# Kernel optimization log

Hardware: AMD Instinct MI355X
Metric: run time of the kernel (lower is better)

## Reference

```python
import jax, jax.numpy as jnp
import numpy as np

N_NODES = 50000
N_EDGES = 1600000
IN_DIM = 128
OUT_DIM = 32
N_HEADS = 4


def setup_inputs() -> dict:
    key = jax.random.key(0)
    k_x, k_e, k_w, k_a = jax.random.split(key, 4)
    x = jax.random.normal(k_x, (N_NODES, IN_DIM), dtype=jnp.float32)
    edge_index = jax.random.randint(k_e, (N_EDGES, 2), 0, N_NODES, dtype=jnp.int64)
    # Xavier-uniform-like init scales
    w_bound = np.sqrt(6.0 / (IN_DIM + OUT_DIM)).astype(np.float32)
    a_bound = np.sqrt(6.0 / (N_HEADS + 2 * OUT_DIM)).astype(np.float32)
    weight = jax.random.uniform(k_w, (N_HEADS, IN_DIM, OUT_DIM), dtype=jnp.float32,
                                minval=-w_bound, maxval=w_bound)
    attn = jax.random.uniform(k_a, (N_HEADS, 2 * OUT_DIM), dtype=jnp.float32,
                              minval=-a_bound, maxval=a_bound)
    return {"x": x, "edge_index": edge_index, "weight": weight, "attn": attn}


def reference(x, edge_index, weight, attn):
    # x: [N, in_dim]; edge_index: [E, 2]; weight: [H, in, out]; attn: [H, 2*out]
    num_nodes = x.shape[0]
    out_dim = weight.shape[2]
    src = edge_index[:, 0]
    dst = edge_index[:, 1]

    # Per-head linear transform: [N, H, out]
    Wh = jnp.einsum('ni,hio->nho', x, weight)
    Wh_src = Wh[src]  # [E, H, out]
    Wh_dst = Wh[dst]  # [E, H, out]

    a_src = attn[:, :out_dim]   # [H, out]
    a_dst = attn[:, out_dim:]   # [H, out]
    # Edge scores: [E, H]
    e = jnp.einsum('eho,ho->eh', Wh_src, a_src) + jnp.einsum('eho,ho->eh', Wh_dst, a_dst)
    e = jax.nn.leaky_relu(e, negative_slope=0.2)

    # Segment softmax over incoming edges of each dst node
    max_per_dst = jax.ops.segment_max(e, dst, num_segments=num_nodes)  # [N, H]
    max_per_dst = jnp.where(jnp.isfinite(max_per_dst), max_per_dst, 0.0)
    exp_e = jnp.exp(e - max_per_dst[dst])                               # [E, H]
    sum_per_dst = jax.ops.segment_sum(exp_e, dst, num_segments=num_nodes)  # [N, H]
    alpha = exp_e / (sum_per_dst[dst] + 1e-9)                           # [E, H]
    # Dropout is identity in eval mode.

    # Weighted scatter-add aggregation: [N, H, out]
    out = jax.ops.segment_sum(alpha[:, :, None] * Wh_src, dst, num_segments=num_nodes)
    h = out.reshape(num_nodes, -1)  # concat heads -> [N, H*out]
    return h, alpha
```

## Files before the change

### kernel.cpp

```cpp
#include <hip/hip_runtime.h>
#include <hip/hip_bf16.h>
#include <math.h>

#define N_NODES 50000
#define N_EDGES 1600000
#define IN_DIM  128
#define OUT_DIM 32
#define N_HEADS 4
#define WH_DIM  (N_HEADS * OUT_DIM)
#define CAP     128
#define NB_SCAN 196
#define NPASS   4
#define WIN     (N_NODES / NPASS)
#define NCH2    32
#define SEGCAP  410000
#define UNROLL  16
#define EPB     (256 * UNROLL)
#define NB_CVT  391
#define NB_WH   782
#define SFLAG   (1 << 30)

typedef __attribute__((ext_vector_type(8))) short short8;
typedef __attribute__((ext_vector_type(4))) float floatx4;

__device__ __forceinline__ short f2bf(float v) {
    __hip_bfloat16 b = __float2bfloat16(v);
    return *reinterpret_cast<short*>(&b);
}
__device__ __forceinline__ float lrelu(float v) {
    return v > 0.0f ? v : 0.2f * v;
}

__device__ __forceinline__ void load_edge(const void* eidx, int is32, int e,
                                          int& s, int& d) {
    if (is32) {
        const int2 v = ((const int2*)eidx)[e];
        s = v.x; d = v.y;
    } else {
        const longlong2 v = ((const longlong2*)eidx)[e];
        s = (int)v.x; d = (int)v.y;
    }
}

__global__ __launch_bounds__(256) void k_prep0(
        const float* __restrict__ weight, const float* __restrict__ attn,
        short* __restrict__ bsw_pre, int* __restrict__ win_cnt,
        int* __restrict__ bsum) {
    __shared__ float ubuf[128 * 8];
    const int t = threadIdx.x;
    if (t < NPASS) win_cnt[t] = 0;
    if (t < NB_SCAN) bsum[t] = 0;
    {
        int c = t & 7, k0 = t >> 3;
        int h = c & 3;
        const float* ap = attn + h * 64 + (c >> 2) * 32;
        for (int k = k0; k < 128; k += 32) {
            const float* wp = weight + h * (IN_DIM * OUT_DIM) + k * OUT_DIM;
            float u = 0.f;
#pragma unroll
            for (int o = 0; o < 32; o += 4) {
                float4 wv = *(const float4*)(wp + o);
                float4 av = *(const float4*)(ap + o);
                u += wv.x * av.x + wv.y * av.y + wv.z * av.z + wv.w * av.w;
            }
            ubuf[k * 8 + c] = u;
        }
    }
    __syncthreads();
    for (int f = t; f < 128 * 128; f += 256) {
        int k = f >> 7, c = f & 127;
        float w = weight[(c >> 5) * (IN_DIM * OUT_DIM) + k * OUT_DIM + (c & 31)];
        int kc = k >> 5, quad = (k >> 3) & 3, j = k & 7;
        bsw_pre[((kc * 9 + (c >> 4)) * 64 + quad * 16 + (c & 15)) * 8 + j] =
            f2bf(w);
    }
    for (int f = t; f < 128 * 16; f += 256) {
        int k = f >> 4, c = f & 15;
        float w = (c < 8) ? ubuf[k * 8 + c] : 0.f;
        int kc = k >> 5, quad = (k >> 3) & 3, j = k & 7;
        bsw_pre[((kc * 9 + 8) * 64 + quad * 16 + c) * 8 + j] = f2bf(w);
    }
}

union CvtWhSmem {
    struct {
        int s_is32;
        int wcnt[NPASS][UNROLL][4];
        int pb[NPASS][UNROLL][4];
        int bw[NPASS];
    } c;
    struct {
        short xsw[4 * 4 * 64 * 8];
        short bsw[4 * 9 * 64 * 8];
    } w;
};

__global__ __launch_bounds__(256) void k_cvtwh(
        const void* __restrict__ eidx, const float* __restrict__ x,
        const short* __restrict__ bsw_pre,
        int* __restrict__ win_cnt, int* __restrict__ win_sd,
        __hip_bfloat16* __restrict__ Wh16, float* __restrict__ sb16) {
    __shared__ CvtWhSmem sm;
    const int t = threadIdx.x;

    if (blockIdx.x < NB_CVT) {
        const int wv = t >> 6, lane = t & 63;
        if (t < 64) {
            int hi = ((const int*)eidx)[2 * (t * 25000) + 1];
            unsigned long long b = __ballot(hi != 0);
            if (t == 0) sm.c.s_is32 = (b != 0ULL) ? 1 : 0;
        }
        __syncthreads();
        const int is32 = sm.c.s_is32;
        const int e0 = blockIdx.x * EPB;
        int sg[UNROLL], dg[UNROLL];
#pragma unroll
        for (int i = 0; i < UNROLL; ++i) {
            const int e = e0 + i * 256 + t;
            int s = 0, d = -1;
            if (e < N_EDGES) load_edge(eidx, is32, e, s, d);
            sg[i] = s; dg[i] = d;
            const int w = (d >= 0) ? (d / WIN) : -1;
            const unsigned long long m0 = __ballot(w == 0);
            const unsigned long long m1 = __ballot(w == 1);
            const unsigned long long m2 = __ballot(w == 2);
            const unsigned long long m3 = __ballot(w == 3);
            if (lane == 0) {
                sm.c.wcnt[0][i][wv] = __popcll(m0);
                sm.c.wcnt[1][i][wv] = __popcll(m1);
                sm.c.wcnt[2][i][wv] = __popcll(m2);
                sm.c.wcnt[3][i][wv] = __popcll(m3);
            }
        }
        __syncthreads();
        if (t < NPASS) {
            int run = 0;
            for (int i = 0; i < UNROLL; ++i)
                for (int v = 0; v < 4; ++v) {
                    sm.c.pb[t][i][v] = run;
                    run += sm.c.wcnt[t][i][v];
                }
            sm.c.bw[t] = atomicAdd(&win_cnt[t], run);
        }
        __syncthreads();
        const unsigned long long mlt = (1ULL << lane) - 1ULL;
#pragma unroll
        for (int i = 0; i < UNROLL; ++i) {
            const int d = dg[i];
            const int w = (d >= 0) ? (d / WIN) : -1;
            const unsigned long long m0 = __ballot(w == 0);
            const unsigned long long m1 = __ballot(w == 1);
            const unsigned long long m2 = __ballot(w == 2);
            const unsigned long long m3 = __ballot(w == 3);
            if (w >= 0) {
                const unsigned long long mw = (w == 0) ? m0 : (w == 1) ? m1
                                            : (w == 2) ? m2 : m3;
                const int rank = __popcll(mw & mlt);
                const int p = sm.c.bw[w] + sm.c.pb[w][i][wv] + rank;
                if (p < SEGCAP)
                    win_sd[w * SEGCAP + p] = sg[i] | ((d - w * WIN) << 17);
            }
        }
    } else {
        const int nb = (blockIdx.x - NB_CVT) * 64;
        for (int f = t; f < 4 * 9 * 64; f += 256)
            *(short8*)&sm.w.bsw[f * 8] = *(const short8*)&bsw_pre[f * 8];
        for (int f = t; f < 64 * 32; f += 256) {
            int n = f >> 5, k = (f & 31) * 4;
            int ng = nb + n; if (ng > N_NODES - 1) ng = N_NODES - 1;
            float4 v = *(const float4*)(x + (size_t)ng * IN_DIM + k);
            int wg = n >> 4, m = n & 15, kc = k >> 5, quad = (k >> 3) & 3,
                j = k & 7;
            short4 sv = make_short4(f2bf(v.x), f2bf(v.y), f2bf(v.z), f2bf(v.w));
            *(short4*)&sm.w.xsw[(((wg * 4 + kc) * 64) + quad * 16 + m) * 8 + j]
                = sv;
        }
        __syncthreads();
        const int wg = t >> 6, lane = t & 63;
        floatx4 acc[9];
#pragma unroll
        for (int i = 0; i < 9; ++i) acc[i] = (floatx4){0.f, 0.f, 0.f, 0.f};
#pragma unroll
        for (int kc = 0; kc < 4; ++kc) {
            short8 a = *(short8*)&sm.w.xsw[((wg * 4 + kc) * 64 + lane) * 8];
#pragma unroll
            for (int cg = 0; cg < 9; ++cg) {
                short8 b = *(short8*)&sm.w.bsw[((kc * 9 + cg) * 64 + lane) * 8];
                acc[cg] = __builtin_amdgcn_mfma_f32_16x16x32_bf16(a, b, acc[cg],
                                                                  0, 0, 0);
            }
        }
        const int col = lane & 15, quad = lane >> 4;
#pragma unroll
        for (int r = 0; r < 4; ++r) {
            int n = nb + wg * 16 + quad * 4 + r;
            if (n >= N_NODES) continue;
#pragma unroll
            for (int cg = 0; cg < 8; ++cg)
                Wh16[(size_t)n * WH_DIM + cg * 16 + col] =
                    __float2bfloat16(acc[cg][r]);
            if (col < 8) sb16[(size_t)n * 16 + col] = acc[8][r];
        }
    }
}

__global__ __launch_bounds__(1024) void k_hist(
        const int* __restrict__ win_cnt, const int* __restrict__ win_sd,
        int* __restrict__ hist) {
    __shared__ int hbin[WIN];
    const int c = blockIdx.x, w = blockIdx.y;
    for (int i = threadIdx.x; i < WIN; i += 1024) hbin[i] = 0;
    __syncthreads();
    const int cw = win_cnt[w];
    const int ce = (cw + NCH2 - 1) / NCH2;
    const int lo = c * ce;
    const int hi = min(lo + ce, cw);
    for (int i = lo + threadIdx.x; i < hi; i += 1024) {
        unsigned u = ((unsigned)win_sd[w * SEGCAP + i]) >> 17;
        if (u < WIN) atomicAdd(&hbin[u], 1);
    }
    __syncthreads();
    for (int i = threadIdx.x; i < WIN; i += 1024)
        hist[(w * NCH2 + c) * WIN + i] = hbin[i];
}

__global__ __launch_bounds__(256) void k_scanbase(
        int* __restrict__ bsum, int* __restrict__ hist,
        int* __restrict__ noff) {
    __shared__ int sh[256];
    const int t = threadIdx.x;
    const int b = blockIdx.x;
    const int i = b * 256 + t;
    int v = 0;
    if (i < N_NODES) {
        const int w = i / WIN, bin = i % WIN;
        for (int c = 0; c < NCH2; ++c) v += hist[(w * NCH2 + c) * WIN + bin];
    }
    sh[t] = v;
    __syncthreads();
    for (int d = 1; d < 256; d <<= 1) {
        int u = (t >= d) ? sh[t - d] : 0;
        __syncthreads();
        sh[t] += u;
        __syncthreads();
    }
    const int myex = sh[t] - v;
    if (t == 255) atomicExch(&bsum[b], sh[255] | SFLAG);
    __syncthreads();
    int bvv = 0;
    if (t < NB_SCAN) {
        int xx;
        do { xx = atomicAdd(&bsum[t], 0); } while (!(xx & SFLAG));
        bvv = xx & ~SFLAG;
    }
    sh[t] = bvv;
    __syncthreads();
    for (int d = 1; d < 256; d <<= 1) {
        int u = (t >= d) ? sh[t - d] : 0;
        __syncthreads();
        sh[t] += u;
        __syncthreads();
    }
    const int exb = (b == 0) ? 0 : sh[b - 1];
    if (b == 0 && t == 0) noff[N_NODES] = N_EDGES;
    if (i >= N_NODES) return;
    int run = myex + exb;
    noff[i] = run;
    const int w = i / WIN, bin = i % WIN;
    for (int c = 0; c < NCH2; ++c) {
        const int idx = (w * NCH2 + c) * WIN + bin;
        int t0 = hist[idx];
        hist[idx] = run;
        run += t0;
    }
}

__global__ __launch_bounds__(1024) void k_scatter(
        const int* __restrict__ win_cnt, const int* __restrict__ win_sd,
        const int* __restrict__ hist, int* __restrict__ csr) {
    __shared__ int pos[WIN];
    const int c = blockIdx.x, w = blockIdx.y;
    for (int i = threadIdx.x; i < WIN; i += 1024)
        pos[i] = hist[(w * NCH2 + c) * WIN + i];
    __syncthreads();
    const int cw = win_cnt[w];
    const int ce = (cw + NCH2 - 1) / NCH2;
    const int lo = c * ce;
    const int hi = min(lo + ce, cw);
    for (int i = lo + threadIdx.x; i < hi; i += 1024) {
        const int pk = win_sd[w * SEGCAP + i];
        const int s = pk & 0x1FFFF;
        const unsigned u = ((unsigned)pk) >> 17;
        if (u < WIN) {
            int p = atomicAdd(&pos[u], 1);
            csr[p] = s;
        }
    }
}

__global__ __launch_bounds__(256) void k_node(
        const int* __restrict__ noff,
        const int* __restrict__ csr, float* __restrict__ sb16,
        const __hip_bfloat16* __restrict__ Wh16,
        float* __restrict__ out_h) {
    __shared__ int    sbuf[4][CAP];
    __shared__ float4 e4b[4][CAP];
    const int wv = threadIdx.x >> 6;
    const int t  = threadIdx.x & 63;
    const int n  = blockIdx.x * 4 + wv;
    const int beg = noff[n];
    const int end = noff[n + 1];
    const int deg = end - beg;

    const float4 sd = *(const float4*)(sb16 + (size_t)n * 16 + 4);

    float4 sum = {0.f, 0.f, 0.f, 0.f};
    for (int l = t; l < deg; l += 64) {
        int s = csr[beg + l];
        float4 ss = *(const float4*)(sb16 + (size_t)s * 16);
        float4 ex;
        ex.x = __expf(lrelu(ss.x + sd.x));
        ex.y = __expf(lrelu(ss.y + sd.y));
        ex.z = __expf(lrelu(ss.z + sd.z));
        ex.w = __expf(lrelu(ss.w + sd.w));
        if (l < CAP) { sbuf[wv][l] = s; e4b[wv][l] = ex; }
        sum.x += ex.x; sum.y += ex.y; sum.z += ex.z; sum.w += ex.w;
    }
#pragma unroll
    for (int o = 32; o; o >>= 1) {
        sum.x += __shfl_xor(sum.x, o);
        sum.y += __shfl_xor(sum.y, o);
        sum.z += __shfl_xor(sum.z, o);
        sum.w += __shfl_xor(sum.w, o);
    }
    float4 inv;
    inv.x = 1.0f / (sum.x + 1e-9f); inv.y = 1.0f / (sum.y + 1e-9f);
    inv.z = 1.0f / (sum.z + 1e-9f); inv.w = 1.0f / (sum.w + 1e-9f);
    if (t == 0) *(float4*)(sb16 + (size_t)n * 16 + 8) = inv;

    const int esl = t >> 4;
    const int dsl = t & 15;
    const int h   = dsl >> 2;
    const float invh = (h == 0) ? inv.x : (h == 1) ? inv.y
                     : (h == 2) ? inv.z : inv.w;
    const float sdh  = (h == 0) ? sd.x : (h == 1) ? sd.y
                     : (h == 2) ? sd.z : sd.w;
    float acc0 = 0.f, acc1 = 0.f, acc2 = 0.f, acc3 = 0.f;
    float acc4 = 0.f, acc5 = 0.f, acc6 = 0.f, acc7 = 0.f;
    if (deg <= CAP) {
        const int sPad = sbuf[wv][0];
        for (int jb = 0; jb < deg; jb += 16) {
            int   sg[4];
            float ag[4];
#pragma unroll
            for (int g = 0; g < 4; ++g) {
                const int idx = jb + g * 4 + esl;
                sg[g] = sPad;
                ag[g] = 0.f;
                if (idx < deg) {
                    sg[g] = sbuf[wv][idx];
                    ag[g] = ((const float*)&e4b[wv][idx])[h];
                }
            }
            uint4 w0 = *(const uint4*)(Wh16 + (size_t)sg[0] * WH_DIM + dsl * 8);
            uint4 w1 = *(const uint4*)(Wh16 + (size_t)sg[1] * WH_DIM + dsl * 8);
            uint4 w2 = *(const uint4*)(Wh16 + (size_t)sg[2] * WH_DIM + dsl * 8);
            uint4 w3 = *(const uint4*)(Wh16 + (size_t)sg[3] * WH_DIM + dsl * 8);
#define ACC8(W, A)                                                            \
            acc0 += (A) * __uint_as_float((W).x << 16);                       \
            acc1 += (A) * __uint_as_float((W).x & 0xffff0000u);               \
            acc2 += (A) * __uint_as_float((W).y << 16);                       \
            acc3 += (A) * __uint_as_float((W).y & 0xffff0000u);               \
            acc4 += (A) * __uint_as_float((W).z << 16);                       \
            acc5 += (A) * __uint_as_float((W).z & 0xffff0000u);               \
            acc6 += (A) * __uint_as_float((W).w << 16);                       \
            acc7 += (A) * __uint_as_float((W).w & 0xffff0000u)
            ACC8(w0, ag[0]);
            ACC8(w1, ag[1]);
            ACC8(w2, ag[2]);
            ACC8(w3, ag[3]);
#undef ACC8
        }
    } else {
        for (int jb = 0; jb < deg; jb += 4) {
            const int idx = jb + esl;
            float a = 0.f;
            int s = sbuf[wv][0];
            if (idx < deg) {
                if (idx < CAP) {
                    s = sbuf[wv][idx];
                    a = ((const float*)&e4b[wv][idx])[h];
                } else {
                    s = csr[beg + idx];
                    a = __expf(lrelu(sb16[(size_t)s * 16 + h] + sdh));
                }
            }
            const uint4 w = *(const uint4*)(Wh16 + (size_t)s * WH_DIM + dsl * 8);
            acc0 += a * __uint_as_float(w.x << 16);
            acc1 += a * __uint_as_float(w.x & 0xffff0000u);
            acc2 += a * __uint_as_float(w.y << 16);
            acc3 += a * __uint_as_float(w.y & 0xffff0000u);
            acc4 += a * __uint_as_float(w.z << 16);
            acc5 += a * __uint_as_float(w.z & 0xffff0000u);
            acc6 += a * __uint_as_float(w.w << 16);
            acc7 += a * __uint_as_float(w.w & 0xffff0000u);
        }
    }
    acc0 += __shfl_xor(acc0, 16); acc0 += __shfl_xor(acc0, 32);
    acc1 += __shfl_xor(acc1, 16); acc1 += __shfl_xor(acc1, 32);
    acc2 += __shfl_xor(acc2, 16); acc2 += __shfl_xor(acc2, 32);
    acc3 += __shfl_xor(acc3, 16); acc3 += __shfl_xor(acc3, 32);
    acc4 += __shfl_xor(acc4, 16); acc4 += __shfl_xor(acc4, 32);
    acc5 += __shfl_xor(acc5, 16); acc5 += __shfl_xor(acc5, 32);
    acc6 += __shfl_xor(acc6, 16); acc6 += __shfl_xor(acc6, 32);
    acc7 += __shfl_xor(acc7, 16); acc7 += __shfl_xor(acc7, 32);
    if (t < 16) {
        float* op = out_h + (size_t)n * WH_DIM + dsl * 8;
        float4 o0 = {acc0 * invh, acc1 * invh, acc2 * invh, acc3 * invh};
        float4 o1 = {acc4 * invh, acc5 * invh, acc6 * invh, acc7 * invh};
        *(float4*)op = o0;
        *(float4*)(op + 4) = o1;
    }
}

__global__ __launch_bounds__(256) void k_alpha(
        const void* __restrict__ eidx,
        const float* __restrict__ sb16, float* __restrict__ ebuf) {
    __shared__ int s_is32;
    const int t = threadIdx.x;
    if (t < 64) {
        int hi = ((const int*)eidx)[2 * (t * 25000) + 1];
        unsigned long long b = __ballot(hi != 0);
        if (t == 0) s_is32 = (b != 0ULL) ? 1 : 0;
    }
    __syncthreads();
    const int e = blockIdx.x * 256 + t;
    int s, d;
    load_edge(eidx, s_is32, e, s, d);
    float4 ss = *(const float4*)(sb16 + (size_t)s * 16);
    float4 sd = *(const float4*)(sb16 + (size_t)d * 16 + 4);
    float4 iv = *(const float4*)(sb16 + (size_t)d * 16 + 8);
    float4 a;
    a.x = __expf(lrelu(ss.x + sd.x)) * iv.x;
    a.y = __expf(lrelu(ss.y + sd.y)) * iv.y;
    a.z = __expf(lrelu(ss.z + sd.z)) * iv.z;
    a.w = __expf(lrelu(ss.w + sd.w)) * iv.w;
    *(float4*)(ebuf + (size_t)e * 4) = a;
}

extern "C" void kernel_launch(void* const* d_in, const int* in_sizes, int n_in,
                              void* d_out, int out_size, void* d_ws, size_t ws_size,
                              hipStream_t stream) {
    const float* x      = (const float*)d_in[0];
    const void*  eidx   = d_in[1];
    const float* weight = (const float*)d_in[2];
    const float* attn   = (const float*)d_in[3];

    float* out   = (float*)d_out;
    float* out_h = out;
    float* ebuf  = out + (size_t)N_NODES * WH_DIM;

    char* ws = (char*)d_ws;
    int*   win_cnt = (int*)ws;
    int*   bsum    = (int*)(ws + 64);
    short* bsw_pre = (short*)(ws + 1024);
    int*   noff    = (int*)(ws + 37952);
    int*   win_sd  = (int*)(ws + 238016);
    int*   hist    = (int*)(ws + 6798080);
    int*   csr     = (int*)(ws + 13198144);
    __hip_bfloat16* Wh16 = (__hip_bfloat16*)(ws + 19598208);
    float* sb16    = (float*)(ws + 32398272);

    k_prep0<<<1, 256, 0, stream>>>(weight, attn, bsw_pre, win_cnt, bsum);
    k_cvtwh<<<NB_CVT + NB_WH, 256, 0, stream>>>(eidx, x, bsw_pre, win_cnt,
                                                win_sd, Wh16, sb16);
    dim3 hg(NCH2, NPASS);
    k_hist<<<hg, 1024, 0, stream>>>(win_cnt, win_sd, hist);
    k_scanbase<<<NB_SCAN, 256, 0, stream>>>(bsum, hist, noff);
    k_scatter<<<hg, 1024, 0, stream>>>(win_cnt, win_sd, hist, csr);
    k_node<<<N_NODES / 4, 256, 0, stream>>>(noff, csr, sb16, Wh16, out_h);
    k_alpha<<<N_EDGES / 256, 256, 0, stream>>>(eidx, sb16, ebuf);
}
```

Before: 253.5 us.

## Fuse histogram, scan and scatter into one persistent kernel with grid barriers

Merges the three counting-sort kernels (histogram, scan, scatter) into a single 128-block persistent kernel that uses atomic global barriers between phases, removing two kernel launches and their gaps. The scan now uses 1024-wide blocks and a simple serial prefix over 49 block sums. The weight-to-bf16 swizzle in the prep kernel is spread across 16 blocks instead of one. The grid barrier relies on all 128 blocks being co-resident, which holds on this GPU but is not guaranteed in general. It also adds spin-wait overhead.

```diff
diff --git a/kernel.cpp b/kernel.cpp
--- a/kernel.cpp
+++ b/kernel.cpp
@@ -9,7 +9,6 @@
 #define N_HEADS 4
 #define WH_DIM  (N_HEADS * OUT_DIM)
 #define CAP     128
-#define NB_SCAN 196
 #define NPASS   4
 #define WIN     (N_NODES / NPASS)
 #define NCH2    32
@@ -18,7 +17,9 @@
 #define EPB     (256 * UNROLL)
 #define NB_CVT  391
 #define NB_WH   782
-#define SFLAG   (1 << 30)
+#define NB_SORT (NCH2 * NPASS)
+#define NB_P2   49
+#define NB_PREP 16
 
 typedef __attribute__((ext_vector_type(8))) short short8;
 typedef __attribute__((ext_vector_type(4))) float floatx4;
@@ -42,14 +43,34 @@
     }
 }
 
+__device__ __forceinline__ void gbar(int* bar, int idx) {
+    __syncthreads();
+    if (threadIdx.x == 0) {
+        __threadfence();
+        atomicAdd(&bar[idx], 1);
+        while (atomicAdd(&bar[idx], 0) < NB_SORT) {}
+        __threadfence();
+    }
+    __syncthreads();
+}
+
 __global__ __launch_bounds__(256) void k_prep0(
         const float* __restrict__ weight, const float* __restrict__ attn,
         short* __restrict__ bsw_pre, int* __restrict__ win_cnt,
-        int* __restrict__ bsum) {
+        int* __restrict__ bar) {
     __shared__ float ubuf[128 * 8];
     const int t = threadIdx.x;
+    const int b = blockIdx.x;
+    for (int f = b * 1024 + t; f < (b + 1) * 1024; f += 256) {
+        int k = f >> 7, c = f & 127;
+        float w = weight[(c >> 5) * (IN_DIM * OUT_DIM) + k * OUT_DIM + (c & 31)];
+        int kc = k >> 5, quad = (k >> 3) & 3, j = k & 7;
+        bsw_pre[((kc * 9 + (c >> 4)) * 64 + quad * 16 + (c & 15)) * 8 + j] =
+            f2bf(w);
+    }
+    if (b != 0) return;
     if (t < NPASS) win_cnt[t] = 0;
-    if (t < NB_SCAN) bsum[t] = 0;
+    if (t < 8) bar[t] = 0;
     {
         int c = t & 7, k0 = t >> 3;
         int h = c & 3;
@@ -67,13 +88,6 @@
         }
     }
     __syncthreads();
-    for (int f = t; f < 128 * 128; f += 256) {
-        int k = f >> 7, c = f & 127;
-        float w = weight[(c >> 5) * (IN_DIM * OUT_DIM) + k * OUT_DIM + (c & 31)];
-        int kc = k >> 5, quad = (k >> 3) & 3, j = k & 7;
-        bsw_pre[((kc * 9 + (c >> 4)) * 64 + quad * 16 + (c & 15)) * 8 + j] =
-            f2bf(w);
-    }
     for (int f = t; f < 128 * 16; f += 256) {
         int k = f >> 4, c = f & 15;
         float w = (c < 8) ? ubuf[k * 8 + c] : 0.f;
@@ -204,96 +218,84 @@
     }
 }
 
-__global__ __launch_bounds__(1024) void k_hist(
+__global__ __launch_bounds__(1024) void k_sort(
         const int* __restrict__ win_cnt, const int* __restrict__ win_sd,
-        int* __restrict__ hist) {
-    __shared__ int hbin[WIN];
-    const int c = blockIdx.x, w = blockIdx.y;
-    for (int i = threadIdx.x; i < WIN; i += 1024) hbin[i] = 0;
+        int* __restrict__ hist, int* __restrict__ bsum2,
+        int* __restrict__ noff, int* __restrict__ csr, int* __restrict__ bar) {
+    __shared__ int lds[WIN];
+    __shared__ int xb;
+    const int bid = blockIdx.x;
+    const int t = threadIdx.x;
+    const int c = bid & (NCH2 - 1), w = bid >> 5;
+    for (int i = t; i < WIN; i += 1024) lds[i] = 0;
     __syncthreads();
     const int cw = win_cnt[w];
     const int ce = (cw + NCH2 - 1) / NCH2;
-    const int lo = c * ce;
-    const int hi = min(lo + ce, cw);
-    for (int i = lo + threadIdx.x; i < hi; i += 1024) {
+    const int lo = c * ce, hi = min(lo + ce, cw);
+    for (int i = lo + t; i < hi; i += 1024) {
         unsigned u = ((unsigned)win_sd[w * SEGCAP + i]) >> 17;
-        if (u < WIN) atomicAdd(&hbin[u], 1);
-    }
-    __syncthreads();
-    for (int i = threadIdx.x; i < WIN; i += 1024)
-        hist[(w * NCH2 + c) * WIN + i] = hbin[i];
-}
-
-__global__ __launch_bounds__(256) void k_scanbase(
-        int* __restrict__ bsum, int* __restrict__ hist,
-        int* __restrict__ noff) {
-    __shared__ int sh[256];
-    const int t = threadIdx.x;
-    const int b = blockIdx.x;
-    const int i = b * 256 + t;
-    int v = 0;
-    if (i < N_NODES) {
-        const int w = i / WIN, bin = i % WIN;
-        for (int c = 0; c < NCH2; ++c) v += hist[(w * NCH2 + c) * WIN + bin];
-    }
-    sh[t] = v;
-    __syncthreads();
-    for (int d = 1; d < 256; d <<= 1) {
-        int u = (t >= d) ? sh[t - d] : 0;
-        __syncthreads();
-        sh[t] += u;
-        __syncthreads();
-    }
-    const int myex = sh[t] - v;
-    if (t == 255) atomicExch(&bsum[b], sh[255] | SFLAG);
-    __syncthreads();
-    int bvv = 0;
-    if (t < NB_SCAN) {
-        int xx;
-        do { xx = atomicAdd(&bsum[t], 0); } while (!(xx & SFLAG));
-        bvv = xx & ~SFLAG;
-    }
-    sh[t] = bvv;
-    __syncthreads();
-    for (int d = 1; d < 256; d <<= 1) {
-        int u = (t >= d) ? sh[t - d] : 0;
-        __syncthreads();
-        sh[t] += u;
-        __syncthreads();
-    }
-    const int exb = (b == 0) ? 0 : sh[b - 1];
-    if (b == 0 && t == 0) noff[N_NODES] = N_EDGES;
-    if (i >= N_NODES) return;
-    int run = myex + exb;
-    noff[i] = run;
-    const int w = i / WIN, bin = i % WIN;
-    for (int c = 0; c < NCH2; ++c) {
-        const int idx = (w * NCH2 + c) * WIN + bin;
-        int t0 = hist[idx];
-        hist[idx] = run;
-        run += t0;
-    }
-}
-
-__global__ __launch_bounds__(1024) void k_scatter(
-        const int* __restrict__ win_cnt, const int* __restrict__ win_sd,
-        const int* __restrict__ hist, int* __restrict__ csr) {
-    __shared__ int pos[WIN];
-    const int c = blockIdx.x, w = blockIdx.y;
-    for (int i = threadIdx.x; i < WIN; i += 1024)
-        pos[i] = hist[(w * NCH2 + c) * WIN + i];
-    __syncthreads();
-    const int cw = win_cnt[w];
-    const int ce = (cw + NCH2 - 1) / NCH2;
-    const int lo = c * ce;
-    const int hi = min(lo + ce, cw);
-    for (int i = lo + threadIdx.x; i < hi; i += 1024) {
+        if (u < WIN) atomicAdd(&lds[u], 1);
+    }
+    __syncthreads();
+    for (int i = t; i < WIN; i += 1024)
+        hist[(w * NCH2 + c) * WIN + i] = lds[i];
+    gbar(bar, 0);
+    int myex = 0, vdeg = 0;
+    if (bid < NB_P2) {
+        const int i = bid * 1024 + t;
+        int v = 0;
+        if (i < N_NODES) {
+            const int w2 = i / WIN, bin = i % WIN;
+            for (int cc = 0; cc < NCH2; ++cc)
+                v += hist[(w2 * NCH2 + cc) * WIN + bin];
+        }
+        vdeg = v;
+        lds[t] = v;
+        __syncthreads();
+        for (int d = 1; d < 1024; d <<= 1) {
+            int u = (t >= d) ? lds[t - d] : 0;
+            __syncthreads();
+            lds[t] += u;
+            __syncthreads();
+        }
+        myex = lds[t] - vdeg;
+        if (t == 1023) bsum2[bid] = lds[1023];
+    }
+    gbar(bar, 1);
+    if (bid < NB_P2) {
+        if (t < NB_P2) lds[t] = bsum2[t];
+        __syncthreads();
+        if (t == 0) {
+            int e = 0;
+            for (int j = 0; j < bid; ++j) e += lds[j];
+            xb = e;
+        }
+        __syncthreads();
+        const int exb = xb;
+        if (bid == 0 && t == 0) noff[N_NODES] = N_EDGES;
+        const int i = bid * 1024 + t;
+        if (i < N_NODES) {
+            int run = myex + exb;
+            noff[i] = run;
+            const int w2 = i / WIN, bin = i % WIN;
+            for (int cc = 0; cc < NCH2; ++cc) {
+                const int idx = (w2 * NCH2 + cc) * WIN + bin;
+                int t0 = hist[idx];
+                hist[idx] = run;
+                run += t0;
+            }
+        }
+    }
+    gbar(bar, 2);
+    for (int i = t; i < WIN; i += 1024)
+        lds[i] = hist[(w * NCH2 + c) * WIN + i];
+    __syncthreads();
+    for (int i = lo + t; i < hi; i += 1024) {
         const int pk = win_sd[w * SEGCAP + i];
-        const int s = pk & 0x1FFFF;
         const unsigned u = ((unsigned)pk) >> 17;
         if (u < WIN) {
-            int p = atomicAdd(&pos[u], 1);
-            csr[p] = s;
+            int p = atomicAdd(&lds[u], 1);
+            csr[p] = pk & 0x1FFFF;
         }
     }
 }
@@ -462,7 +464,8 @@
 
     char* ws = (char*)d_ws;
     int*   win_cnt = (int*)ws;
-    int*   bsum    = (int*)(ws + 64);
+    int*   bar     = (int*)(ws + 64);
+    int*   bsum2   = (int*)(ws + 128);
     short* bsw_pre = (short*)(ws + 1024);
     int*   noff    = (int*)(ws + 37952);
     int*   win_sd  = (int*)(ws + 238016);
@@ -471,13 +474,11 @@
     __hip_bfloat16* Wh16 = (__hip_bfloat16*)(ws + 19598208);
     float* sb16    = (float*)(ws + 32398272);
 
-    k_prep0<<<1, 256, 0, stream>>>(weight, attn, bsw_pre, win_cnt, bsum);
+    k_prep0<<<NB_PREP, 256, 0, stream>>>(weight, attn, bsw_pre, win_cnt, bar);
     k_cvtwh<<<NB_CVT + NB_WH, 256, 0, stream>>>(eidx, x, bsw_pre, win_cnt,
                                                 win_sd, Wh16, sb16);
-    dim3 hg(NCH2, NPASS);
-    k_hist<<<hg, 1024, 0, stream>>>(win_cnt, win_sd, hist);
-    k_scanbase<<<NB_SCAN, 256, 0, stream>>>(bsum, hist, noff);
-    k_scatter<<<hg, 1024, 0, stream>>>(win_cnt, win_sd, hist, csr);
+    k_sort<<<NB_SORT, 1024, 0, stream>>>(win_cnt, win_sd, hist, bsum2,
+                                         noff, csr, bar);
     k_node<<<N_NODES / 4, 256, 0, stream>>>(noff, csr, sb16, Wh16, out_h);
     k_alpha<<<N_EDGES / 256, 256, 0, stream>>>(eidx, sb16, ebuf);
 }
```

Result: slower. 276.5 us (+9.1%).
